# Kernel tuning notes

Measured on AMD Instinct MI355X. Metric: run time of the kernel, lower is better.

Reference implementation:

```python
import jax, jax.numpy as jnp
import numpy as np

B, C, H, W = 4, 512, 128, 128   # batch, in_channels, feature map HxW
KC = 256                        # key_channels
KP = 150                        # number of proxy regions (ADE20K classes)


def conv1x1(x, w, b):
    # x: [b,c,h,w], w: [k,c], b: [k] -> [b,k,h,w]
    return jnp.einsum('bchw,kc->bkhw', x, w) + b[None, :, None, None]


def proj2(x, w1, b1, w2, b2):
    # conv1x1-(BN folded)-relu twice, as in f_pixel / f_object
    h = jax.nn.relu(conv1x1(x, w1, b1))
    return jax.nn.relu(conv1x1(h, w2, b2))


def setup_inputs() -> dict:
    key = jax.random.key(0)
    ks = jax.random.split(key, 16)
    nrm = lambda k, shape, s=0.05: (jax.random.normal(k, shape, jnp.float32) * s)
    return {
        'x': jax.random.normal(ks[0], (B, C, H, W), jnp.float32),
        'proxy_feats': jax.random.normal(ks[1], (B, C, KP, 1), jnp.float32),
        # f_pixel: two 1x1 convs (BN in eval mode folded into weight+bias)
        'w_p1': nrm(ks[2], (KC, C)), 'b_p1': nrm(ks[3], (KC,)),
        'w_p2': nrm(ks[4], (KC, KC)), 'b_p2': nrm(ks[5], (KC,)),
        # f_object
        'w_o1': nrm(ks[6], (KC, C)), 'b_o1': nrm(ks[7], (KC,)),
        'w_o2': nrm(ks[8], (KC, KC)), 'b_o2': nrm(ks[9], (KC,)),
        # f_down
        'w_d': nrm(ks[10], (KC, C)), 'b_d': nrm(ks[11], (KC,)),
        # f_up
        'w_u': nrm(ks[12], (C, KC)), 'b_u': nrm(ks[13], (C,)),
    }


def reference(x, proxy_feats, w_p1, b_p1, w_p2, b_p2, w_o1, b_o1, w_o2, b_o2,
              w_d, b_d, w_u, b_u):
    b, _, h, w = x.shape
    n = h * w
    # query: [b, n, kc]
    query = proj2(x, w_p1, b_p1, w_p2, b_p2).reshape(b, KC, n).transpose(0, 2, 1)
    # key: [b, kc, kp]
    k = proj2(proxy_feats, w_o1, b_o1, w_o2, b_o2).reshape(b, KC, KP)
    # value: [b, kp, kc]
    v = jax.nn.relu(conv1x1(proxy_feats, w_d, b_d)).reshape(b, KC, KP).transpose(0, 2, 1)
    # scaled dot-product cross-attention
    sim = jnp.einsum('bnc,bck->bnk', query, k) * (KC ** -0.5)
    sim = jax.nn.softmax(sim, axis=-1)
    context = jnp.einsum('bnk,bkc->bnc', sim, v)            # [b, n, kc]
    context = context.transpose(0, 2, 1).reshape(b, KC, h, w)
    return jax.nn.relu(conv1x1(context, w_u, b_u))           # [b, C, h, w]
```

## Files before the change

### kernel.cpp

```cpp
#include <hip/hip_runtime.h>
#include <hip/hip_bf16.h>

#define NB   4
#define CIN  512
#define NPX  16384
#define KC   256
#define KP   150
#define KVP  192

typedef __attribute__((ext_vector_type(8))) short short8;
typedef __attribute__((ext_vector_type(4))) float f32x4;
typedef __attribute__((ext_vector_type(4))) unsigned int u32x4;
typedef unsigned short u16;

__device__ __forceinline__ u16 f2bf(float f) {
    unsigned int u = __float_as_uint(f);
    return (u16)((u + 0x7FFFu + ((u >> 16) & 1u)) >> 16);
}
__device__ __forceinline__ unsigned pk2(float a, float b) {
    return (unsigned)f2bf(a) | ((unsigned)f2bf(b) << 16);
}
__device__ __forceinline__ void gload_lds16(const void* g, void* l) {
    __builtin_amdgcn_global_load_lds(
        (const __attribute__((address_space(1))) unsigned int*)g,
        (__attribute__((address_space(3))) unsigned int*)l,
        16, 0, 0);
}
__device__ __forceinline__ int swz8(int c, int r7) { return (c & ~7) | ((c & 7) ^ r7); }

__global__ __launch_bounds__(512, 2)
void fused_kernel(const u16* __restrict__ wp1, const float* __restrict__ xg,
                  const u16* __restrict__ wp2, const float* __restrict__ bp1,
                  const float* __restrict__ bp2, const u16* __restrict__ keyg,
                  const u16* __restrict__ vtg, const u16* __restrict__ wug,
                  const float* __restrict__ bu, float* __restrict__ outg)
{
    __shared__ u16 sh[73728];

    const int b  = blockIdx.z;
    const int n0 = blockIdx.x * 128;
    const int tid = threadIdx.x, lane = tid & 63, wid = tid >> 6;
    const int rg = lane & 15, kg = lane >> 4;
    const int r7 = rg & 7;
    const int mg = wid >> 1, ng = wid & 1;

    const float* xb = xg + (long)b * CIN * NPX;
    const u16* kyb  = keyg + (long)b * 160 * KC;
    const u16* vb   = vtg + (long)b * KC * KVP;
    float* ob       = outg + (long)b * CIN * NPX;

    const int sxn = tid & 127, sxk = tid >> 7;
    const float* xsrc = xb + (long)(sxk * 16) * NPX + n0 + sxn;

    auto STAGE_WA = [&](int buf, int kt) {
        #pragma unroll
        for (int it = 0; it < 4; ++it) {
            int idx = it * 512 + tid;
            int row = idx >> 3, c = idx & 7;
            gload_lds16(wp1 + (long)row * CIN + (kt * 8 + (c ^ (row & 7))) * 8,
                        sh + buf * 16384 + (it * 512 + wid * 64) * 8);
        }
    };
    float xr[16];
    auto LOADX = [&](int kt) {
        #pragma unroll
        for (int e = 0; e < 16; ++e)
            xr[e] = xsrc[(long)(kt * 64 + e) * NPX];
    };
    auto WRITE_XB = [&](int buf) {
        #pragma unroll
        for (int h = 0; h < 2; ++h) {
            u32x4 v;
            v.x = pk2(xr[h * 8 + 0], xr[h * 8 + 1]);
            v.y = pk2(xr[h * 8 + 2], xr[h * 8 + 3]);
            v.z = pk2(xr[h * 8 + 4], xr[h * 8 + 5]);
            v.w = pk2(xr[h * 8 + 6], xr[h * 8 + 7]);
            int p = (sxk * 2 + h) ^ (sxn & 7);
            *(u32x4*)(sh + 32768 + buf * 8192 + sxn * 64 + p * 8) = v;
        }
    };

    STAGE_WA(0, 0); LOADX(0); WRITE_XB(0);
    __syncthreads();

    f32x4 acc[4][4];
    #pragma unroll
    for (int i = 0; i < 4; ++i)
        #pragma unroll
        for (int j = 0; j < 4; ++j) acc[i][j] = (f32x4){0.f, 0.f, 0.f, 0.f};

    for (int kt = 0; kt < 8; ++kt) {
        const int buf = kt & 1;
        if (kt < 7) { STAGE_WA(buf ^ 1, kt + 1); LOADX(kt + 1); }
        #pragma unroll
        for (int s = 0; s < 2; ++s) {
            const int cc = (4 * s + kg) ^ r7;
            short8 a[4], bb[4];
            #pragma unroll
            for (int i = 0; i < 4; ++i)
                a[i] = *(const short8*)(sh + buf * 16384 + (mg * 64 + i * 16 + rg) * 64 + cc * 8);
            #pragma unroll
            for (int j = 0; j < 4; ++j)
                bb[j] = *(const short8*)(sh + 32768 + buf * 8192 + (ng * 64 + j * 16 + rg) * 64 + cc * 8);
            #pragma unroll
            for (int i = 0; i < 4; ++i)
                #pragma unroll
                for (int j = 0; j < 4; ++j)
                    acc[i][j] = __builtin_amdgcn_mfma_f32_16x16x32_bf16(a[i], bb[j], acc[i][j], 0, 0, 0);
        }
        if (kt < 7) WRITE_XB(buf ^ 1);
        __syncthreads();
    }

    #pragma unroll
    for (int i = 0; i < 4; ++i) {
        const int kc = mg * 64 + i * 16 + kg * 4;
        const f32x4 bv = *(const f32x4*)(bp1 + kc);
        const int c = mg * 8 + 2 * i + (kg >> 1);
        #pragma unroll
        for (int j = 0; j < 4; ++j) {
            const int n = ng * 64 + j * 16 + rg;
            uint2 pk;
            pk.x = pk2(fmaxf(acc[i][j][0] + bv.x, 0.f), fmaxf(acc[i][j][1] + bv.y, 0.f));
            pk.y = pk2(fmaxf(acc[i][j][2] + bv.z, 0.f), fmaxf(acc[i][j][3] + bv.w, 0.f));
            *(uint2*)(sh + n * 256 + swz8(c, r7) * 8 + (kg & 1) * 4) = pk;
        }
    }

    auto STAGE_W2 = [&](int buf, int S) {
        #pragma unroll
        for (int it = 0; it < 2; ++it) {
            int idx = it * 512 + tid;
            int row = idx >> 2, c = idx & 3;
            gload_lds16(wp2 + (long)row * KC + (S * 4 + (c ^ (row & 3))) * 8,
                        sh + 32768 + buf * 8192 + (it * 512 + wid * 64) * 8);
        }
    };
    STAGE_W2(0, 0);
    __syncthreads();

    f32x4 acc2[4][4];
    #pragma unroll
    for (int i = 0; i < 4; ++i)
        #pragma unroll
        for (int j = 0; j < 4; ++j) acc2[i][j] = (f32x4){0.f, 0.f, 0.f, 0.f};

    for (int S = 0; S < 8; ++S) {
        const int buf = S & 1;
        if (S < 7) STAGE_W2(buf ^ 1, S + 1);
        short8 a[4], bb[4];
        #pragma unroll
        for (int i = 0; i < 4; ++i)
            a[i] = *(const short8*)(sh + 32768 + buf * 8192 + (mg * 64 + i * 16 + rg) * 32 + (kg ^ (rg & 3)) * 8);
        #pragma unroll
        for (int j = 0; j < 4; ++j)
            bb[j] = *(const short8*)(sh + (ng * 64 + j * 16 + rg) * 256 + swz8(S * 4 + kg, r7) * 8);
        #pragma unroll
        for (int i = 0; i < 4; ++i)
            #pragma unroll
            for (int j = 0; j < 4; ++j)
                acc2[i][j] = __builtin_amdgcn_mfma_f32_16x16x32_bf16(a[i], bb[j], acc2[i][j], 0, 0, 0);
        __syncthreads();
    }

    #pragma unroll
    for (int i = 0; i < 4; ++i) {
        const int kc = mg * 64 + i * 16 + kg * 4;
        const f32x4 bv = *(const f32x4*)(bp2 + kc);
        const int c = mg * 8 + 2 * i + (kg >> 1);
        #pragma unroll
        for (int j = 0; j < 4; ++j) {
            const int n = ng * 64 + j * 16 + rg;
            uint2 pk;
            pk.x = pk2(fmaxf(acc2[i][j][0] + bv.x, 0.f), fmaxf(acc2[i][j][1] + bv.y, 0.f));
            pk.y = pk2(fmaxf(acc2[i][j][2] + bv.z, 0.f), fmaxf(acc2[i][j][3] + bv.w, 0.f));
            *(uint2*)(sh + 40960 + n * 256 + swz8(c, r7) * 8 + (kg & 1) * 4) = pk;
        }
    }
    #pragma unroll
    for (int it = 0; it < 8; ++it) {
        int idx = it * 512 + tid;
        int row = idx >> 5, c = idx & 31;
        gload_lds16(kyb + (long)row * KC + swz8(c, row & 7) * 8,
                    sh + (it * 512 + wid * 64) * 8);
    }
    #pragma unroll
    for (int it = 0; it < 2; ++it) {
        int idx = it * 512 + tid;
        int row = 128 + (idx >> 5), c = idx & 31;
        gload_lds16(kyb + (long)row * KC + swz8(c, row & 7) * 8,
                    sh + 32768 + (it * 512 + wid * 64) * 8);
    }
    __syncthreads();

    f32x4 s1[10];
    #pragma unroll
    for (int i = 0; i < 10; ++i) s1[i] = (f32x4){0.f, 0.f, 0.f, 0.f};
    for (int s = 0; s < 8; ++s) {
        const int cc = swz8(4 * s + kg, r7);
        short8 bq = *(const short8*)(sh + 40960 + (wid * 16 + rg) * 256 + cc * 8);
        #pragma unroll
        for (int i = 0; i < 10; ++i) {
            const u16* krow = (i < 8) ? (sh + (i * 16 + rg) * 256)
                                      : (sh + 32768 + ((i - 8) * 16 + rg) * 256);
            short8 a = *(const short8*)(krow + cc * 8);
            s1[i] = __builtin_amdgcn_mfma_f32_16x16x32_bf16(a, bq, s1[i], 0, 0, 0);
        }
    }
    float mx = -3.0e38f;
    #pragma unroll
    for (int i = 0; i < 9; ++i)
        #pragma unroll
        for (int r = 0; r < 4; ++r) mx = fmaxf(mx, s1[i][r]);
    #pragma unroll
    for (int r = 0; r < 4; ++r) if (kg * 4 + r < 6) mx = fmaxf(mx, s1[9][r]);
    mx = fmaxf(mx, __shfl_xor(mx, 16));
    mx = fmaxf(mx, __shfl_xor(mx, 32));
    float l = 0.f;
    #pragma unroll
    for (int i = 0; i < 10; ++i)
        #pragma unroll
        for (int r = 0; r < 4; ++r) {
            const bool valid = (i < 9) || (kg * 4 + r < 6);
            float e = valid ? __expf((s1[i][r] - mx) * 0.0625f) : 0.f;
            s1[i][r] = e; l += e;
        }
    l += __shfl_xor(l, 16);
    l += __shfl_xor(l, 32);
    const float inv = 1.f / l;

    __syncthreads();

    #pragma unroll
    for (int i = 0; i < 10; ++i) {
        uint2 pk;
        pk.x = pk2(s1[i][0] * inv, s1[i][1] * inv);
        pk.y = pk2(s1[i][2] * inv, s1[i][3] * inv);
        const int c = 2 * i + (kg >> 1);
        *(uint2*)(sh + (wid * 16 + rg) * KVP + swz8(c, r7) * 8 + (kg & 1) * 4) = pk;
    }
    #pragma unroll
    for (int it = 0; it < 12; ++it) {
        int idx = it * 512 + tid;
        int row = idx / 24, c = idx - row * 24;
        gload_lds16(vb + (long)row * KVP + swz8(c, row & 7) * 8,
                    sh + 24576 + (it * 512 + wid * 64) * 8);
    }
    __syncthreads();

    f32x4 acc4[4][4];
    #pragma unroll
    for (int i = 0; i < 4; ++i)
        #pragma unroll
        for (int j = 0; j < 4; ++j) acc4[i][j] = (f32x4){0.f, 0.f, 0.f, 0.f};
    for (int s = 0; s < 5; ++s) {
        const int cc = swz8(4 * s + kg, r7);
        short8 a[4], bb[4];
        #pragma unroll
        for (int i = 0; i < 4; ++i)
            a[i] = *(const short8*)(sh + 24576 + (mg * 64 + i * 16 + rg) * KVP + cc * 8);
        #pragma unroll
        for (int j = 0; j < 4; ++j)
            bb[j] = *(const short8*)(sh + (ng * 64 + j * 16 + rg) * KVP + cc * 8);
        #pragma unroll
        for (int i = 0; i < 4; ++i)
            #pragma unroll
            for (int j = 0; j < 4; ++j)
                acc4[i][j] = __builtin_amdgcn_mfma_f32_16x16x32_bf16(a[i], bb[j], acc4[i][j], 0, 0, 0);
    }
    __syncthreads();

    #pragma unroll
    for (int i = 0; i < 4; ++i) {
        const int c = mg * 8 + 2 * i + (kg >> 1);
        #pragma unroll
        for (int j = 0; j < 4; ++j) {
            const int n = ng * 64 + j * 16 + rg;
            uint2 pk;
            pk.x = pk2(acc4[i][j][0], acc4[i][j][1]);
            pk.y = pk2(acc4[i][j][2], acc4[i][j][3]);
            *(uint2*)(sh + n * 256 + swz8(c, r7) * 8 + (kg & 1) * 4) = pk;
        }
    }
    auto STAGE_WU = [&](int buf, int S) {
        #pragma unroll
        for (int it = 0; it < 4; ++it) {
            int idx = it * 512 + tid;
            int row = idx >> 2, c = idx & 3;
            gload_lds16(wug + (long)row * KC + (S * 4 + (c ^ (row & 3))) * 8,
                        sh + 32768 + buf * 16384 + (it * 512 + wid * 64) * 8);
        }
    };
    STAGE_WU(0, 0);
    __syncthreads();

    f32x4 acc5[8][4];
    #pragma unroll
    for (int i = 0; i < 8; ++i)
        #pragma unroll
        for (int j = 0; j < 4; ++j) acc5[i][j] = (f32x4){0.f, 0.f, 0.f, 0.f};
    for (int S = 0; S < 8; ++S) {
        const int buf = S & 1;
        if (S < 7) STAGE_WU(buf ^ 1, S + 1);
        short8 bb[4];
        #pragma unroll
        for (int j = 0; j < 4; ++j)
            bb[j] = *(const short8*)(sh + (ng * 64 + j * 16 + rg) * 256 + swz8(S * 4 + kg, r7) * 8);
        #pragma unroll
        for (int i = 0; i < 8; ++i) {
            short8 a = *(const short8*)(sh + 32768 + buf * 16384 + (mg * 128 + i * 16 + rg) * 32 + (kg ^ (rg & 3)) * 8);
            #pragma unroll
            for (int j = 0; j < 4; ++j)
                acc5[i][j] = __builtin_amdgcn_mfma_f32_16x16x32_bf16(a, bb[j], acc5[i][j], 0, 0, 0);
        }
        __syncthreads();
    }

    #pragma unroll
    for (int i = 0; i < 8; ++i) {
        const int c4 = mg * 128 + i * 16 + kg * 4;
        const f32x4 bv = *(const f32x4*)(bu + c4);
        #pragma unroll
        for (int j = 0; j < 4; ++j) {
            const int n = n0 + ng * 64 + j * 16 + rg;
            ob[(long)(c4 + 0) * NPX + n] = fmaxf(acc5[i][j][0] + bv.x, 0.f);
            ob[(long)(c4 + 1) * NPX + n] = fmaxf(acc5[i][j][1] + bv.y, 0.f);
            ob[(long)(c4 + 2) * NPX + n] = fmaxf(acc5[i][j][2] + bv.z, 0.f);
            ob[(long)(c4 + 3) * NPX + n] = fmaxf(acc5[i][j][3] + bv.w, 0.f);
        }
    }
}

__global__ void kv1_kernel(const float* __restrict__ proxy,
                           const float* __restrict__ w_o1, const float* __restrict__ b_o1,
                           const float* __restrict__ w_d,  const float* __restrict__ b_d,
                           float* __restrict__ hidden, u16* __restrict__ vT)
{
    const int kc = blockIdx.x;
    const int b  = blockIdx.y;
    const int kp = threadIdx.x;
    float ah = 0.f, av = 0.f;
    if (kp < KP) {
        const float* px = proxy + (long)b * CIN * KP + kp;
        const float* w1 = w_o1 + (long)kc * CIN;
        const float* wd = w_d  + (long)kc * CIN;
        for (int c = 0; c < CIN; ++c) {
            float p = px[(long)c * KP];
            ah += w1[c] * p;
            av += wd[c] * p;
        }
        ah = fmaxf(ah + b_o1[kc], 0.f);
        av = fmaxf(av + b_d[kc], 0.f);
    }
    if (kp < 160) hidden[((long)b * KC + kc) * 160 + kp] = ah;
    vT[((long)b * KC + kc) * KVP + kp] = f2bf(av);
}

__global__ void kv2_kernel(const float* __restrict__ hidden,
                           const float* __restrict__ w_o2, const float* __restrict__ b_o2,
                           u16* __restrict__ keyT)
{
    const int kp = blockIdx.x;
    const int b  = blockIdx.y;
    const int kc = threadIdx.x;
    long o = ((long)b * 160 + kp) * KC + kc;
    if (kp >= KP) { keyT[o] = 0; return; }
    const float* w = w_o2 + (long)kc * KC;
    const float* h = hidden + (long)b * KC * 160 + kp;
    float acc = 0.f;
    for (int c = 0; c < KC; ++c)
        acc += w[c] * h[(long)c * 160];
    keyT[o] = f2bf(fmaxf(acc + b_o2[kc], 0.f));
}

__global__ void prep_w(const float* __restrict__ w1, const float* __restrict__ w2,
                       const float* __restrict__ w3,
                       u16* __restrict__ o1, u16* __restrict__ o2, u16* __restrict__ o3)
{
    int i = blockIdx.x * 256 + threadIdx.x;
    if (i < KC * CIN) o1[i] = f2bf(w1[i]);
    if (i < KC * KC)  o2[i] = f2bf(w2[i]);
    if (i < CIN * KC) o3[i] = f2bf(w3[i]);
}

extern "C" void kernel_launch(void* const* d_in, const int* in_sizes, int n_in,
                              void* d_out, int out_size, void* d_ws, size_t ws_size,
                              hipStream_t stream)
{
    const float* x     = (const float*)d_in[0];
    const float* proxy = (const float*)d_in[1];
    const float* w_p1  = (const float*)d_in[2];
    const float* b_p1  = (const float*)d_in[3];
    const float* w_p2  = (const float*)d_in[4];
    const float* b_p2  = (const float*)d_in[5];
    const float* w_o1  = (const float*)d_in[6];
    const float* b_o1  = (const float*)d_in[7];
    const float* w_o2  = (const float*)d_in[8];
    const float* b_o2  = (const float*)d_in[9];
    const float* w_d   = (const float*)d_in[10];
    const float* b_d   = (const float*)d_in[11];
    const float* w_u   = (const float*)d_in[12];
    const float* b_u   = (const float*)d_in[13];
    float* out = (float*)d_out;
    (void)in_sizes; (void)n_in; (void)out_size; (void)ws_size;

    char* ws = (char*)d_ws;
    size_t off = 0;
    auto alloc = [&](size_t bytes) { size_t o = off; off += (bytes + 255) & ~(size_t)255; return o; };

    u16*   wb_p1  = (u16*)  (ws + alloc((size_t)KC * CIN * 2));
    u16*   wb_p2  = (u16*)  (ws + alloc((size_t)KC * KC * 2));
    u16*   wb_u   = (u16*)  (ws + alloc((size_t)CIN * KC * 2));
    u16*   keyT   = (u16*)  (ws + alloc((size_t)NB * 160 * KC * 2));
    u16*   vT     = (u16*)  (ws + alloc((size_t)NB * KC * KVP * 2));
    float* hidden = (float*)(ws + alloc((size_t)NB * KC * 160 * 4));

    prep_w<<<512, 256, 0, stream>>>(w_p1, w_p2, w_u, wb_p1, wb_p2, wb_u);
    kv1_kernel<<<dim3(KC, NB), KVP, 0, stream>>>(proxy, w_o1, b_o1, w_d, b_d, hidden, vT);
    kv2_kernel<<<dim3(160, NB), 256, 0, stream>>>(hidden, w_o2, b_o2, keyT);

    fused_kernel<<<dim3(NPX / 128, 1, NB), 512, 0, stream>>>(
        wb_p1, x, wb_p2, b_p1, b_p2, keyT, vT, wb_u, b_u, out);
}
```

Measured before the change: 159.4 us.

## Pre-pack weights and K/V into MFMA fragment order, read directly from global

Weights, key and value are pre-packed on the host-side prep kernels into MFMA fragment order, so the fused kernel loads A operands straight from global memory (L2-resident) instead of staging them through LDS. This shrinks shared memory from 144KB to about 66KB, allowing higher occupancy (launch bounds 4), and uses padded strides instead of XOR swizzles. The up-projection is split into two halves to reduce register pressure, and the kv1/kv2 precompute kernels are restructured for more reuse. The risk is higher global/L2 traffic and latency on A-fragment loads without double-buffering.

```diff
diff --git a/kernel.cpp b/kernel.cpp
--- a/kernel.cpp
+++ b/kernel.cpp
@@ -6,7 +6,12 @@
 #define NPX  16384
 #define KC   256
 #define KP   150
-#define KVP  192
+
+#define LDH  264
+#define LDP  200
+#define LDX  72
+#define SHSZ 33792
+#define XBOF 15360
 
 typedef __attribute__((ext_vector_type(8))) short short8;
 typedef __attribute__((ext_vector_type(4))) float f32x4;
@@ -20,47 +25,34 @@
 __device__ __forceinline__ unsigned pk2(float a, float b) {
     return (unsigned)f2bf(a) | ((unsigned)f2bf(b) << 16);
 }
-__device__ __forceinline__ void gload_lds16(const void* g, void* l) {
-    __builtin_amdgcn_global_load_lds(
-        (const __attribute__((address_space(1))) unsigned int*)g,
-        (__attribute__((address_space(3))) unsigned int*)l,
-        16, 0, 0);
-}
-__device__ __forceinline__ int swz8(int c, int r7) { return (c & ~7) | ((c & 7) ^ r7); }
-
-__global__ __launch_bounds__(512, 2)
-void fused_kernel(const u16* __restrict__ wp1, const float* __restrict__ xg,
-                  const u16* __restrict__ wp2, const float* __restrict__ bp1,
-                  const float* __restrict__ bp2, const u16* __restrict__ keyg,
-                  const u16* __restrict__ vtg, const u16* __restrict__ wug,
+__device__ __forceinline__ short8 ldfrag(const u16* __restrict__ p, int idx) {
+    return *(const short8*)(p + ((long)idx << 3));
+}
+
+__global__ __launch_bounds__(512, 4)
+void fused_kernel(const u16* __restrict__ wp1p, const float* __restrict__ xg,
+                  const u16* __restrict__ wp2p, const float* __restrict__ bp1,
+                  const float* __restrict__ bp2, const u16* __restrict__ keyp,
+                  const u16* __restrict__ vp, const u16* __restrict__ wup,
                   const float* __restrict__ bu, float* __restrict__ outg)
 {
-    __shared__ u16 sh[73728];
+    __shared__ u16 sh[SHSZ];
 
     const int b  = blockIdx.z;
     const int n0 = blockIdx.x * 128;
     const int tid = threadIdx.x, lane = tid & 63, wid = tid >> 6;
     const int rg = lane & 15, kg = lane >> 4;
-    const int r7 = rg & 7;
     const int mg = wid >> 1, ng = wid & 1;
 
     const float* xb = xg + (long)b * CIN * NPX;
-    const u16* kyb  = keyg + (long)b * 160 * KC;
-    const u16* vb   = vtg + (long)b * KC * KVP;
     float* ob       = outg + (long)b * CIN * NPX;
+    const u16* kyp  = keyp + (long)b * 40960;
+    const u16* vbp  = vp   + (long)b * 40960;
 
     const int sxn = tid & 127, sxk = tid >> 7;
     const float* xsrc = xb + (long)(sxk * 16) * NPX + n0 + sxn;
-
-    auto STAGE_WA = [&](int buf, int kt) {
-        #pragma unroll
-        for (int it = 0; it < 4; ++it) {
-            int idx = it * 512 + tid;
-            int row = idx >> 3, c = idx & 7;
-            gload_lds16(wp1 + (long)row * CIN + (kt * 8 + (c ^ (row & 7))) * 8,
-                        sh + buf * 16384 + (it * 512 + wid * 64) * 8);
-        }
-    };
+    u16* XB = sh + XBOF;
+
     float xr[16];
     auto LOADX = [&](int kt) {
         #pragma unroll
@@ -75,33 +67,31 @@
             v.y = pk2(xr[h * 8 + 2], xr[h * 8 + 3]);
             v.z = pk2(xr[h * 8 + 4], xr[h * 8 + 5]);
             v.w = pk2(xr[h * 8 + 6], xr[h * 8 + 7]);
-            int p = (sxk * 2 + h) ^ (sxn & 7);
-            *(u32x4*)(sh + 32768 + buf * 8192 + sxn * 64 + p * 8) = v;
+            *(u32x4*)(XB + buf * 9216 + sxn * LDX + (sxk * 2 + h) * 8) = v;
         }
     };
 
-    STAGE_WA(0, 0); LOADX(0); WRITE_XB(0);
-    __syncthreads();
-
     f32x4 acc[4][4];
     #pragma unroll
     for (int i = 0; i < 4; ++i)
         #pragma unroll
         for (int j = 0; j < 4; ++j) acc[i][j] = (f32x4){0.f, 0.f, 0.f, 0.f};
+
+    LOADX(0); WRITE_XB(0);
+    __syncthreads();
 
     for (int kt = 0; kt < 8; ++kt) {
         const int buf = kt & 1;
-        if (kt < 7) { STAGE_WA(buf ^ 1, kt + 1); LOADX(kt + 1); }
+        if (kt < 7) LOADX(kt + 1);
         #pragma unroll
         for (int s = 0; s < 2; ++s) {
-            const int cc = (4 * s + kg) ^ r7;
             short8 a[4], bb[4];
             #pragma unroll
             for (int i = 0; i < 4; ++i)
-                a[i] = *(const short8*)(sh + buf * 16384 + (mg * 64 + i * 16 + rg) * 64 + cc * 8);
+                a[i] = ldfrag(wp1p, ((mg * 4 + i) * 16 + kt * 2 + s) * 64 + lane);
             #pragma unroll
             for (int j = 0; j < 4; ++j)
-                bb[j] = *(const short8*)(sh + 32768 + buf * 8192 + (ng * 64 + j * 16 + rg) * 64 + cc * 8);
+                bb[j] = *(const short8*)(XB + buf * 9216 + (ng * 64 + j * 16 + rg) * LDX + (s * 4 + kg) * 8);
             #pragma unroll
             for (int i = 0; i < 4; ++i)
                 #pragma unroll
@@ -114,29 +104,17 @@
 
     #pragma unroll
     for (int i = 0; i < 4; ++i) {
-        const int kc = mg * 64 + i * 16 + kg * 4;
-        const f32x4 bv = *(const f32x4*)(bp1 + kc);
-        const int c = mg * 8 + 2 * i + (kg >> 1);
+        const int kc4 = mg * 64 + i * 16 + kg * 4;
+        const f32x4 bv = *(const f32x4*)(bp1 + kc4);
         #pragma unroll
         for (int j = 0; j < 4; ++j) {
             const int n = ng * 64 + j * 16 + rg;
             uint2 pk;
             pk.x = pk2(fmaxf(acc[i][j][0] + bv.x, 0.f), fmaxf(acc[i][j][1] + bv.y, 0.f));
             pk.y = pk2(fmaxf(acc[i][j][2] + bv.z, 0.f), fmaxf(acc[i][j][3] + bv.w, 0.f));
-            *(uint2*)(sh + n * 256 + swz8(c, r7) * 8 + (kg & 1) * 4) = pk;
-        }
-    }
-
-    auto STAGE_W2 = [&](int buf, int S) {
-        #pragma unroll
-        for (int it = 0; it < 2; ++it) {
-            int idx = it * 512 + tid;
-            int row = idx >> 2, c = idx & 3;
-            gload_lds16(wp2 + (long)row * KC + (S * 4 + (c ^ (row & 3))) * 8,
-                        sh + 32768 + buf * 8192 + (it * 512 + wid * 64) * 8);
-        }
-    };
-    STAGE_W2(0, 0);
+            *(uint2*)(sh + n * LDH + kc4) = pk;
+        }
+    }
     __syncthreads();
 
     f32x4 acc2[4][4];
@@ -146,50 +124,33 @@
         for (int j = 0; j < 4; ++j) acc2[i][j] = (f32x4){0.f, 0.f, 0.f, 0.f};
 
     for (int S = 0; S < 8; ++S) {
-        const int buf = S & 1;
-        if (S < 7) STAGE_W2(buf ^ 1, S + 1);
         short8 a[4], bb[4];
         #pragma unroll
         for (int i = 0; i < 4; ++i)
-            a[i] = *(const short8*)(sh + 32768 + buf * 8192 + (mg * 64 + i * 16 + rg) * 32 + (kg ^ (rg & 3)) * 8);
+            a[i] = ldfrag(wp2p, ((mg * 4 + i) * 8 + S) * 64 + lane);
         #pragma unroll
         for (int j = 0; j < 4; ++j)
-            bb[j] = *(const short8*)(sh + (ng * 64 + j * 16 + rg) * 256 + swz8(S * 4 + kg, r7) * 8);
+            bb[j] = *(const short8*)(sh + (ng * 64 + j * 16 + rg) * LDH + S * 32 + kg * 8);
         #pragma unroll
         for (int i = 0; i < 4; ++i)
             #pragma unroll
             for (int j = 0; j < 4; ++j)
                 acc2[i][j] = __builtin_amdgcn_mfma_f32_16x16x32_bf16(a[i], bb[j], acc2[i][j], 0, 0, 0);
-        __syncthreads();
-    }
+    }
+    __syncthreads();
 
     #pragma unroll
     for (int i = 0; i < 4; ++i) {
-        const int kc = mg * 64 + i * 16 + kg * 4;
-        const f32x4 bv = *(const f32x4*)(bp2 + kc);
-        const int c = mg * 8 + 2 * i + (kg >> 1);
+        const int kc4 = mg * 64 + i * 16 + kg * 4;
+        const f32x4 bv = *(const f32x4*)(bp2 + kc4);
         #pragma unroll
         for (int j = 0; j < 4; ++j) {
             const int n = ng * 64 + j * 16 + rg;
             uint2 pk;
             pk.x = pk2(fmaxf(acc2[i][j][0] + bv.x, 0.f), fmaxf(acc2[i][j][1] + bv.y, 0.f));
             pk.y = pk2(fmaxf(acc2[i][j][2] + bv.z, 0.f), fmaxf(acc2[i][j][3] + bv.w, 0.f));
-            *(uint2*)(sh + 40960 + n * 256 + swz8(c, r7) * 8 + (kg & 1) * 4) = pk;
-        }
-    }
-    #pragma unroll
-    for (int it = 0; it < 8; ++it) {
-        int idx = it * 512 + tid;
-        int row = idx >> 5, c = idx & 31;
-        gload_lds16(kyb + (long)row * KC + swz8(c, row & 7) * 8,
-                    sh + (it * 512 + wid * 64) * 8);
-    }
-    #pragma unroll
-    for (int it = 0; it < 2; ++it) {
-        int idx = it * 512 + tid;
-        int row = 128 + (idx >> 5), c = idx & 31;
-        gload_lds16(kyb + (long)row * KC + swz8(c, row & 7) * 8,
-                    sh + 32768 + (it * 512 + wid * 64) * 8);
+            *(uint2*)(sh + n * LDH + kc4) = pk;
+        }
     }
     __syncthreads();
 
@@ -197,13 +158,10 @@
     #pragma unroll
     for (int i = 0; i < 10; ++i) s1[i] = (f32x4){0.f, 0.f, 0.f, 0.f};
     for (int s = 0; s < 8; ++s) {
-        const int cc = swz8(4 * s + kg, r7);
-        short8 bq = *(const short8*)(sh + 40960 + (wid * 16 + rg) * 256 + cc * 8);
+        short8 bq = *(const short8*)(sh + (wid * 16 + rg) * LDH + s * 32 + kg * 8);
         #pragma unroll
         for (int i = 0; i < 10; ++i) {
-            const u16* krow = (i < 8) ? (sh + (i * 16 + rg) * 256)
-                                      : (sh + 32768 + ((i - 8) * 16 + rg) * 256);
-            short8 a = *(const short8*)(krow + cc * 8);
+            short8 a = ldfrag(kyp, (i * 8 + s) * 64 + lane);
             s1[i] = __builtin_amdgcn_mfma_f32_16x16x32_bf16(a, bq, s1[i], 0, 0, 0);
         }
     }
@@ -228,7 +186,6 @@
     l += __shfl_xor(l, 16);
     l += __shfl_xor(l, 32);
     const float inv = 1.f / l;
-
     __syncthreads();
 
     #pragma unroll
@@ -236,15 +193,7 @@
         uint2 pk;
         pk.x = pk2(s1[i][0] * inv, s1[i][1] * inv);
         pk.y = pk2(s1[i][2] * inv, s1[i][3] * inv);
-        const int c = 2 * i + (kg >> 1);
-        *(uint2*)(sh + (wid * 16 + rg) * KVP + swz8(c, r7) * 8 + (kg & 1) * 4) = pk;
-    }
-    #pragma unroll
-    for (int it = 0; it < 12; ++it) {
-        int idx = it * 512 + tid;
-        int row = idx / 24, c = idx - row * 24;
-        gload_lds16(vb + (long)row * KVP + swz8(c, row & 7) * 8,
-                    sh + 24576 + (it * 512 + wid * 64) * 8);
+        *(uint2*)(sh + (wid * 16 + rg) * LDP + i * 16 + kg * 4) = pk;
     }
     __syncthreads();
 
@@ -254,14 +203,13 @@
         #pragma unroll
         for (int j = 0; j < 4; ++j) acc4[i][j] = (f32x4){0.f, 0.f, 0.f, 0.f};
     for (int s = 0; s < 5; ++s) {
-        const int cc = swz8(4 * s + kg, r7);
         short8 a[4], bb[4];
         #pragma unroll
         for (int i = 0; i < 4; ++i)
-            a[i] = *(const short8*)(sh + 24576 + (mg * 64 + i * 16 + rg) * KVP + cc * 8);
+            a[i] = ldfrag(vbp, ((mg * 4 + i) * 5 + s) * 64 + lane);
         #pragma unroll
         for (int j = 0; j < 4; ++j)
-            bb[j] = *(const short8*)(sh + (ng * 64 + j * 16 + rg) * KVP + cc * 8);
+            bb[j] = *(const short8*)(sh + (ng * 64 + j * 16 + rg) * LDP + s * 32 + kg * 8);
         #pragma unroll
         for (int i = 0; i < 4; ++i)
             #pragma unroll
@@ -272,115 +220,139 @@
 
     #pragma unroll
     for (int i = 0; i < 4; ++i) {
-        const int c = mg * 8 + 2 * i + (kg >> 1);
+        const int kc4 = mg * 64 + i * 16 + kg * 4;
         #pragma unroll
         for (int j = 0; j < 4; ++j) {
             const int n = ng * 64 + j * 16 + rg;
             uint2 pk;
             pk.x = pk2(acc4[i][j][0], acc4[i][j][1]);
             pk.y = pk2(acc4[i][j][2], acc4[i][j][3]);
-            *(uint2*)(sh + n * 256 + swz8(c, r7) * 8 + (kg & 1) * 4) = pk;
-        }
-    }
-    auto STAGE_WU = [&](int buf, int S) {
-        #pragma unroll
-        for (int it = 0; it < 4; ++it) {
-            int idx = it * 512 + tid;
-            int row = idx >> 2, c = idx & 3;
-            gload_lds16(wug + (long)row * KC + (S * 4 + (c ^ (row & 3))) * 8,
-                        sh + 32768 + buf * 16384 + (it * 512 + wid * 64) * 8);
-        }
-    };
-    STAGE_WU(0, 0);
-    __syncthreads();
-
-    f32x4 acc5[8][4];
-    #pragma unroll
-    for (int i = 0; i < 8; ++i)
-        #pragma unroll
-        for (int j = 0; j < 4; ++j) acc5[i][j] = (f32x4){0.f, 0.f, 0.f, 0.f};
-    for (int S = 0; S < 8; ++S) {
-        const int buf = S & 1;
-        if (S < 7) STAGE_WU(buf ^ 1, S + 1);
-        short8 bb[4];
-        #pragma unroll
-        for (int j = 0; j < 4; ++j)
-            bb[j] = *(const short8*)(sh + (ng * 64 + j * 16 + rg) * 256 + swz8(S * 4 + kg, r7) * 8);
-        #pragma unroll
-        for (int i = 0; i < 8; ++i) {
-            short8 a = *(const short8*)(sh + 32768 + buf * 16384 + (mg * 128 + i * 16 + rg) * 32 + (kg ^ (rg & 3)) * 8);
+            *(uint2*)(sh + n * LDH + kc4) = pk;
+        }
+    }
+    __syncthreads();
+
+    #pragma unroll 1
+    for (int h2 = 0; h2 < 2; ++h2) {
+        f32x4 a5[4][4];
+        #pragma unroll
+        for (int i = 0; i < 4; ++i)
+            #pragma unroll
+            for (int j = 0; j < 4; ++j) a5[i][j] = (f32x4){0.f, 0.f, 0.f, 0.f};
+        for (int S = 0; S < 8; ++S) {
+            short8 a[4], bb[4];
+            #pragma unroll
+            for (int i = 0; i < 4; ++i)
+                a[i] = ldfrag(wup, ((h2 * 16 + mg * 4 + i) * 8 + S) * 64 + lane);
             #pragma unroll
             for (int j = 0; j < 4; ++j)
-                acc5[i][j] = __builtin_amdgcn_mfma_f32_16x16x32_bf16(a, bb[j], acc5[i][j], 0, 0, 0);
-        }
-        __syncthreads();
-    }
-
-    #pragma unroll
-    for (int i = 0; i < 8; ++i) {
-        const int c4 = mg * 128 + i * 16 + kg * 4;
-        const f32x4 bv = *(const f32x4*)(bu + c4);
-        #pragma unroll
-        for (int j = 0; j < 4; ++j) {
-            const int n = n0 + ng * 64 + j * 16 + rg;
-            ob[(long)(c4 + 0) * NPX + n] = fmaxf(acc5[i][j][0] + bv.x, 0.f);
-            ob[(long)(c4 + 1) * NPX + n] = fmaxf(acc5[i][j][1] + bv.y, 0.f);
-            ob[(long)(c4 + 2) * NPX + n] = fmaxf(acc5[i][j][2] + bv.z, 0.f);
-            ob[(long)(c4 + 3) * NPX + n] = fmaxf(acc5[i][j][3] + bv.w, 0.f);
-        }
-    }
-}
-
-__global__ void kv1_kernel(const float* __restrict__ proxy,
-                           const float* __restrict__ w_o1, const float* __restrict__ b_o1,
-                           const float* __restrict__ w_d,  const float* __restrict__ b_d,
-                           float* __restrict__ hidden, u16* __restrict__ vT)
-{
-    const int kc = blockIdx.x;
-    const int b  = blockIdx.y;
-    const int kp = threadIdx.x;
-    float ah = 0.f, av = 0.f;
-    if (kp < KP) {
-        const float* px = proxy + (long)b * CIN * KP + kp;
-        const float* w1 = w_o1 + (long)kc * CIN;
-        const float* wd = w_d  + (long)kc * CIN;
-        for (int c = 0; c < CIN; ++c) {
-            float p = px[(long)c * KP];
-            ah += w1[c] * p;
-            av += wd[c] * p;
-        }
-        ah = fmaxf(ah + b_o1[kc], 0.f);
-        av = fmaxf(av + b_d[kc], 0.f);
-    }
-    if (kp < 160) hidden[((long)b * KC + kc) * 160 + kp] = ah;
-    vT[((long)b * KC + kc) * KVP + kp] = f2bf(av);
-}
-
-__global__ void kv2_kernel(const float* __restrict__ hidden,
-                           const float* __restrict__ w_o2, const float* __restrict__ b_o2,
-                           u16* __restrict__ keyT)
-{
-    const int kp = blockIdx.x;
-    const int b  = blockIdx.y;
-    const int kc = threadIdx.x;
-    long o = ((long)b * 160 + kp) * KC + kc;
-    if (kp >= KP) { keyT[o] = 0; return; }
-    const float* w = w_o2 + (long)kc * KC;
-    const float* h = hidden + (long)b * KC * 160 + kp;
-    float acc = 0.f;
-    for (int c = 0; c < KC; ++c)
-        acc += w[c] * h[(long)c * 160];
-    keyT[o] = f2bf(fmaxf(acc + b_o2[kc], 0.f));
-}
-
-__global__ void prep_w(const float* __restrict__ w1, const float* __restrict__ w2,
-                       const float* __restrict__ w3,
-                       u16* __restrict__ o1, u16* __restrict__ o2, u16* __restrict__ o3)
-{
-    int i = blockIdx.x * 256 + threadIdx.x;
-    if (i < KC * CIN) o1[i] = f2bf(w1[i]);
-    if (i < KC * KC)  o2[i] = f2bf(w2[i]);
-    if (i < CIN * KC) o3[i] = f2bf(w3[i]);
+                bb[j] = *(const short8*)(sh + (ng * 64 + j * 16 + rg) * LDH + S * 32 + kg * 8);
+            #pragma unroll
+            for (int i = 0; i < 4; ++i)
+                #pragma unroll
+                for (int j = 0; j < 4; ++j)
+                    a5[i][j] = __builtin_amdgcn_mfma_f32_16x16x32_bf16(a[i], bb[j], a5[i][j], 0, 0, 0);
+        }
+        #pragma unroll
+        for (int i = 0; i < 4; ++i) {
+            const int c4 = h2 * 256 + mg * 64 + i * 16 + kg * 4;
+            const f32x4 bv = *(const f32x4*)(bu + c4);
+            #pragma unroll
+            for (int j = 0; j < 4; ++j) {
+                const int n = n0 + ng * 64 + j * 16 + rg;
+                ob[(long)(c4 + 0) * NPX + n] = fmaxf(a5[i][j][0] + bv.x, 0.f);
+                ob[(long)(c4 + 1) * NPX + n] = fmaxf(a5[i][j][1] + bv.y, 0.f);
+                ob[(long)(c4 + 2) * NPX + n] = fmaxf(a5[i][j][2] + bv.z, 0.f);
+                ob[(long)(c4 + 3) * NPX + n] = fmaxf(a5[i][j][3] + bv.w, 0.f);
+            }
+        }
+    }
+}
+
+__global__ __launch_bounds__(192)
+void kv1_kernel(const float* __restrict__ proxy,
+                const float* __restrict__ w_o1, const float* __restrict__ b_o1,
+                const float* __restrict__ w_d,  const float* __restrict__ b_d,
+                float* __restrict__ hiddenT, u16* __restrict__ vp)
+{
+    const int kc0 = blockIdx.x * 4;
+    const int b   = blockIdx.y;
+    const int kp  = threadIdx.x;
+    float ah[4] = {0.f, 0.f, 0.f, 0.f}, av[4] = {0.f, 0.f, 0.f, 0.f};
+    const float* px = proxy + (long)b * CIN * KP + (kp < KP ? kp : 0);
+    for (int c = 0; c < CIN; ++c) {
+        const float p = px[(long)c * KP];
+        #pragma unroll
+        for (int q = 0; q < 4; ++q) {
+            ah[q] += w_o1[(long)(kc0 + q) * CIN + c] * p;
+            av[q] += w_d [(long)(kc0 + q) * CIN + c] * p;
+        }
+    }
+    if (kp < 160) {
+        #pragma unroll
+        for (int q = 0; q < 4; ++q) {
+            const int kc = kc0 + q;
+            const float hv = (kp < KP) ? fmaxf(ah[q] + b_o1[kc], 0.f) : 0.f;
+            const float vv = (kp < KP) ? fmaxf(av[q] + b_d[kc], 0.f) : 0.f;
+            hiddenT[((long)b * 160 + kp) * KC + kc] = hv;
+            const int idx = (((kc >> 4) * 5 + (kp >> 5)) * 64 +
+                             ((kp >> 3) & 3) * 16 + (kc & 15)) * 8 + (kp & 7);
+            vp[(long)b * 40960 + idx] = f2bf(vv);
+        }
+    }
+}
+
+__global__ __launch_bounds__(256)
+void kv2_kernel(const float* __restrict__ hiddenT, const float* __restrict__ wo2T,
+                const float* __restrict__ b_o2, u16* __restrict__ keyp)
+{
+    __shared__ float hl[8][KC];
+    const int kp0 = blockIdx.x * 8;
+    const int b   = blockIdx.y;
+    const int kc  = threadIdx.x;
+    #pragma unroll
+    for (int q = 0; q < 8; ++q)
+        hl[q][kc] = hiddenT[((long)b * 160 + kp0 + q) * KC + kc];
+    __syncthreads();
+    float acc[8] = {0.f, 0.f, 0.f, 0.f, 0.f, 0.f, 0.f, 0.f};
+    for (int c = 0; c < KC; ++c) {
+        const float w = wo2T[(long)c * KC + kc];
+        #pragma unroll
+        for (int q = 0; q < 8; ++q) acc[q] += w * hl[q][c];
+    }
+    const float bb = b_o2[kc];
+    #pragma unroll
+    for (int q = 0; q < 8; ++q) {
+        const int kp = kp0 + q;
+        const float v = (kp < KP) ? fmaxf(acc[q] + bb, 0.f) : 0.f;
+        const int idx = (((kp >> 4) * 8 + (kc >> 5)) * 64 +
+                         ((kc >> 3) & 3) * 16 + (kp & 15)) * 8 + (kc & 7);
+        keyp[(long)b * 40960 + idx] = f2bf(v);
+    }
+}
+
+__global__ __launch_bounds__(256)
+void prep_w(const float* __restrict__ w_p1, const float* __restrict__ w_p2,
+            const float* __restrict__ w_u,  const float* __restrict__ w_o2,
+            u16* __restrict__ wp1p, u16* __restrict__ wp2p,
+            u16* __restrict__ wup, float* __restrict__ wo2T)
+{
+    const int i = blockIdx.x * 256 + threadIdx.x;
+    const int j = i & 7, l = (i >> 3) & 63;
+    {
+        const int S = (i >> 9) & 15, R = i >> 13;
+        wp1p[i] = f2bf(w_p1[(long)(R * 16 + (l & 15)) * CIN + S * 32 + ((l >> 4) << 3) + j]);
+    }
+    {
+        const int S = (i >> 9) & 7, R = i >> 12;
+        wup[i] = f2bf(w_u[(long)(R * 16 + (l & 15)) * KC + S * 32 + ((l >> 4) << 3) + j]);
+    }
+    if (i < 65536) {
+        const int S = (i >> 9) & 7, R = i >> 12;
+        wp2p[i] = f2bf(w_p2[(long)(R * 16 + (l & 15)) * KC + S * 32 + ((l >> 4) << 3) + j]);
+        const int c = i >> 8, kc = i & 255;
+        wo2T[i] = w_o2[(long)kc * KC + c];
+    }
 }
 
 extern "C" void kernel_launch(void* const* d_in, const int* in_sizes, int n_in,
@@ -408,17 +380,18 @@
     size_t off = 0;
     auto alloc = [&](size_t bytes) { size_t o = off; off += (bytes + 255) & ~(size_t)255; return o; };
 
-    u16*   wb_p1  = (u16*)  (ws + alloc((size_t)KC * CIN * 2));
-    u16*   wb_p2  = (u16*)  (ws + alloc((size_t)KC * KC * 2));
-    u16*   wb_u   = (u16*)  (ws + alloc((size_t)CIN * KC * 2));
-    u16*   keyT   = (u16*)  (ws + alloc((size_t)NB * 160 * KC * 2));
-    u16*   vT     = (u16*)  (ws + alloc((size_t)NB * KC * KVP * 2));
-    float* hidden = (float*)(ws + alloc((size_t)NB * KC * 160 * 4));
-
-    prep_w<<<512, 256, 0, stream>>>(w_p1, w_p2, w_u, wb_p1, wb_p2, wb_u);
-    kv1_kernel<<<dim3(KC, NB), KVP, 0, stream>>>(proxy, w_o1, b_o1, w_d, b_d, hidden, vT);
-    kv2_kernel<<<dim3(160, NB), 256, 0, stream>>>(hidden, w_o2, b_o2, keyT);
+    u16*   wp1p    = (u16*)  (ws + alloc((size_t)131072 * 2));
+    u16*   wp2p    = (u16*)  (ws + alloc((size_t)65536 * 2));
+    u16*   wup     = (u16*)  (ws + alloc((size_t)131072 * 2));
+    float* wo2T    = (float*)(ws + alloc((size_t)65536 * 4));
+    u16*   keyp    = (u16*)  (ws + alloc((size_t)NB * 40960 * 2));
+    u16*   vp      = (u16*)  (ws + alloc((size_t)NB * 40960 * 2));
+    float* hiddenT = (float*)(ws + alloc((size_t)NB * 160 * KC * 4));
+
+    prep_w<<<512, 256, 0, stream>>>(w_p1, w_p2, w_u, w_o2, wp1p, wp2p, wup, wo2T);
+    kv1_kernel<<<dim3(64, NB), 192, 0, stream>>>(proxy, w_o1, b_o1, w_d, b_d, hiddenT, vp);
+    kv2_kernel<<<dim3(20, NB), 256, 0, stream>>>(hiddenT, wo2T, b_o2, keyp);
 
     fused_kernel<<<dim3(NPX / 128, 1, NB), 512, 0, stream>>>(
-        wb_p1, x, wb_p2, b_p1, b_p2, keyT, vT, wb_u, b_u, out);
-}
+        wp1p, x, wp2p, b_p1, b_p2, keyp, vp, wup, b_u, out);
+}
```

New measurement: 308.6 us. 1.94x slower.
